# Performance work log

Hardware: AMD Instinct MI355X
Metric: run time of the kernel (lower is better)

## Reference

```python
import jax, jax.numpy as jnp
import numpy as np

NC = 512   # number of symbols / clusters
K = 5      # symbolic conv kernel
S = 2      # symbolic conv stride


def _patches(img, k, s):
    """Extract kxk windows with stride s. img: (H,W) or (H,W,C) int symbols.
    Returns (oh, ow, k, k[, C])."""
    H, W = img.shape[0], img.shape[1]
    oh = (H - k) // s + 1
    ow = (W - k) // s + 1
    hi = jnp.arange(oh) * s
    wi = jnp.arange(ow) * s
    r = img[hi[:, None, None, None] + jnp.arange(k)[None, None, :, None],
            wi[None, :, None, None] + jnp.arange(k)[None, None, None, :]]
    return r, oh, ow


def _sym_conv(sym_img, weights, conv_lut, add_lut):
    """Symbolic conv: per-window gather into conv_lut, sort symbols, then
    sequential left-fold through add_lut (as in SymConv2D).
    sym_img: (H,W) or (H,W,C) int symbols; weights: (L, F) with L=k*k*C."""
    win, oh, ow = _patches(sym_img, K, S)
    if win.ndim == 5:  # (oh,ow,k,k,C) -> channel-major per-window vector (matches reshape(w//C, h*C))
        win = jnp.moveaxis(win, -1, 2)  # (oh,ow,C,k,k)
    win = win.reshape(oh * ow, -1)                      # (n, L)
    prod = conv_lut[win[:, None, :], weights.T[None, :, :]]  # (n, F, L)
    srt = jnp.sort(prod, axis=-1)
    xs = jnp.moveaxis(srt[..., 1:], -1, 0)              # (L-1, n, F)

    def step(carry, s):
        return add_lut[s, carry], None

    out, _ = jax.lax.scan(step, srt[..., 0], xs)        # (n, F)
    return out.reshape(oh, ow, -1)


def _forward_one(x, centroid_lut, W1, W2, W3, conv_lut, add_lut, relu_lut, c1_w, c2_w):
    # discretize: nearest-centroid symbol per 1x1 patch (emulates faiss index)
    sym = jnp.argmin(jnp.abs(x[..., None] - centroid_lut[None, None, :]), axis=-1)  # (28,28)
    h = _sym_conv(sym, c1_w, conv_lut, add_lut)   # (12,12,8)
    h = relu_lut[h]
    h = _sym_conv(h, c2_w, conv_lut, add_lut)     # (4,4,16)
    h = relu_lut[h]
    v = centroid_lut[h]                           # symbolic -> real, (4,4,16)
    v = jnp.transpose(v, (2, 0, 1)).reshape(-1)   # permute(2,0,1).reshape(256)
    a = jax.nn.relu(v @ W1.T)
    a = jax.nn.relu(a @ W2.T)
    return jax.nn.softmax(a @ W3.T)


def setup_inputs() -> dict:
    key = jax.random.key(0)
    ks = jax.random.split(key, 10)
    B = 2048
    return {
        "x_bat": jax.random.uniform(ks[0], (B, 1, 28, 28), jnp.float32),
        "centroid_lut": jax.random.normal(ks[1], (NC,), jnp.float32),
        "W1": jax.random.normal(ks[2], (128, 256), jnp.float32) * 0.06,
        "W2": jax.random.normal(ks[3], (64, 128), jnp.float32) * 0.09,
        "W3": jax.random.normal(ks[4], (10, 64), jnp.float32) * 0.12,
        "conv_lut": jax.random.randint(ks[5], (NC, NC), 0, NC, jnp.int32),
        "add_lut": jax.random.randint(ks[6], (NC, NC), 0, NC, jnp.int32),
        "relu_lut": jax.random.randint(ks[7], (NC,), 0, NC, jnp.int32),
        "c1_weights": jax.random.randint(ks[8], (25, 8), 0, NC, jnp.int32),
        "c2_weights": jax.random.randint(ks[9], (200, 16), 0, NC, jnp.int32),
    }


def reference(x_bat, centroid_lut, W1, W2, W3, conv_lut, add_lut, relu_lut,
              c1_weights, c2_weights):
    f = lambda img: _forward_one(img, centroid_lut, W1, W2, W3,
                                 conv_lut, add_lut, relu_lut,
                                 c1_weights, c2_weights)
    return jax.vmap(f)(x_bat[:, 0])  # (B, 10)
```

## Files before the change

kernel.cpp:

```cpp
#include <hip/hip_runtime.h>


__global__ __launch_bounds__(256) void k_prep(const int* __restrict__ conv_lut,
                                              const int* __restrict__ add_lut,
                                              const int* __restrict__ relu_lut,
                                              unsigned short* __restrict__ lutT,
                                              unsigned short* __restrict__ add16,
                                              unsigned short* __restrict__ relu16) {
  int id = blockIdx.x * 256 + threadIdx.x;
  int s = id >> 9, c = id & 511;
  lutT[c * 512 + s] = (unsigned short)conv_lut[id];
  add16[id] = (unsigned short)add_lut[id];
  if (id < 512) relu16[id] = (unsigned short)relu_lut[id];
}

__global__ __launch_bounds__(256) void k_quant(const float* __restrict__ x,
                                               const float* __restrict__ cen,
                                               unsigned short* __restrict__ sym) {
  __shared__ float cs[512];
  int t = threadIdx.x;
  cs[t] = cen[t];
  cs[t + 256] = cen[t + 256];
  __syncthreads();
  int pix = blockIdx.x * 256 + t;
  float xv = x[pix];
  float bd = 1e30f;
  int bi = 0;
  #pragma unroll 8
  for (int j = 0; j < 512; ++j) {
    float d = fabsf(xv - cs[j]);
    if (d < bd) { bd = d; bi = j; }
  }
  sym[pix] = (unsigned short)bi;
}

__global__ __launch_bounds__(64) void k_conv1(const unsigned short* __restrict__ sym,
                                              const int* __restrict__ c1w,
                                              const unsigned short* __restrict__ lutT,
                                              const unsigned short* __restrict__ add16,
                                              const unsigned short* __restrict__ relu16,
                                              unsigned short* __restrict__ h1) {
  int bid = blockIdx.x;
  int f = bid / 4608;
  int chunk = bid - f * 4608;
  int W = chunk * 64 + threadIdx.x;
  int i = W / 144;
  int p = W - i * 144;
  int wr = p / 12;
  int wc = p - wr * 12;
  const unsigned short* sp = sym + i * 784 + (2 * wr) * 28 + 2 * wc;

  unsigned v[32];
  #pragma unroll
  for (int kh = 0; kh < 5; ++kh)
    #pragma unroll
    for (int kw = 0; kw < 5; ++kw) {
      int l = kh * 5 + kw;
      unsigned sy = sp[kh * 28 + kw];
      int wt = c1w[l * 8 + f];
      v[l] = lutT[((unsigned)wt << 9) + sy];
    }
  #pragma unroll
  for (int l = 25; l < 32; ++l) v[l] = 0xFFFFFFFFu;

  #pragma unroll
  for (int k = 2; k <= 32; k <<= 1) {
    #pragma unroll
    for (int j = k >> 1; j > 0; j >>= 1) {
      #pragma unroll
      for (int a = 0; a < 32; ++a) {
        int b = a ^ j;
        if (b > a) {
          unsigned x0 = v[a], x1 = v[b];
          unsigned lo = min(x0, x1), hi = max(x0, x1);
          bool up = ((a & k) == 0);
          v[a] = up ? lo : hi;
          v[b] = up ? hi : lo;
        }
      }
    }
  }

  unsigned carry = v[0];
  #pragma unroll 1
  for (int l = 1; l < 25; ++l)
    carry = add16[(v[l] << 9) + carry];
  h1[((i * 8 + f) * 12 + wr) * 12 + wc] = relu16[carry];
}

__global__ __launch_bounds__(64) void k_conv2(const unsigned short* __restrict__ h1,
                                              const int* __restrict__ c2w,
                                              const unsigned short* __restrict__ lutT,
                                              const unsigned short* __restrict__ add16,
                                              const unsigned short* __restrict__ relu16,
                                              unsigned short* __restrict__ h2) {
  __shared__ unsigned hist[64][64];
  int lane = threadIdx.x;
  int bid = blockIdx.x;
  int f = bid >> 9;
  int chunk = bid & 511;
  int W = chunk * 64 + lane;
  int i = W >> 4;
  int p = W & 15;
  int wr = p >> 2, wc = p & 3;

  #pragma unroll
  for (int w = 0; w < 64; ++w) hist[w][lane] = 0;

  #pragma unroll 1
  for (int c = 0; c < 8; ++c) {
    int base = ((i * 8 + c) * 12 + 2 * wr) * 12 + 2 * wc;
    #pragma unroll
    for (int kh = 0; kh < 5; ++kh)
      #pragma unroll
      for (int kw = 0; kw < 5; ++kw) {
        unsigned sy = h1[base + kh * 12 + kw];
        int wt = c2w[(c * 25 + kh * 5 + kw) * 16 + f];
        unsigned prod = lutT[((unsigned)wt << 9) + sy];
        hist[prod >> 3][lane] += 1u << ((prod & 7) << 2);
      }
  }

  int wptr = 0;
  unsigned cur = hist[0][lane];
  while (cur == 0 && wptr < 63) { ++wptr; cur = hist[wptr][lane]; }
  unsigned tz = __builtin_ctz(cur);
  unsigned nb = tz >> 2;
  unsigned carry = wptr * 8 + nb;
  cur -= 1u << (nb << 2);
  #pragma unroll 1
  for (int j = 1; j < 200; ++j) {
    while (cur == 0 && wptr < 63) { ++wptr; cur = hist[wptr][lane]; }
    tz = __builtin_ctz(cur);
    nb = tz >> 2;
    unsigned s = wptr * 8 + nb;
    cur -= 1u << (nb << 2);
    carry = add16[(s << 9) + carry];
  }
  h2[((i * 16 + f) * 4 + wr) * 4 + wc] = relu16[carry];
}

__global__ __launch_bounds__(128) void k_mlp(const unsigned short* __restrict__ h2,
                                             const float* __restrict__ cen,
                                             const float* __restrict__ W1,
                                             const float* __restrict__ W2,
                                             const float* __restrict__ W3,
                                             float* __restrict__ out) {
  __shared__ float v[256];
  __shared__ float a1[128];
  __shared__ float a2[64];
  __shared__ float lg[10];
  int i = blockIdx.x, t = threadIdx.x;
  v[t] = cen[h2[i * 256 + t]];
  v[t + 128] = cen[h2[i * 256 + t + 128]];
  __syncthreads();
  float acc = 0.f;
  #pragma unroll 4
  for (int k = 0; k < 256; ++k) acc = fmaf(W1[t * 256 + k], v[k], acc);
  a1[t] = fmaxf(acc, 0.f);
  __syncthreads();
  if (t < 64) {
    acc = 0.f;
    #pragma unroll 4
    for (int k = 0; k < 128; ++k) acc = fmaf(W2[t * 128 + k], a1[k], acc);
    a2[t] = fmaxf(acc, 0.f);
  }
  __syncthreads();
  if (t < 10) {
    acc = 0.f;
    #pragma unroll
    for (int k = 0; k < 64; ++k) acc = fmaf(W3[t * 64 + k], a2[k], acc);
    lg[t] = acc;
  }
  __syncthreads();
  if (t < 10) {
    float m = lg[0];
    #pragma unroll
    for (int j = 1; j < 10; ++j) m = fmaxf(m, lg[j]);
    float ssum = 0.f;
    #pragma unroll
    for (int j = 0; j < 10; ++j) ssum += expf(lg[j] - m);
    out[i * 10 + t] = expf(lg[t] - m) / ssum;
  }
}

extern "C" void kernel_launch(void* const* d_in, const int* in_sizes, int n_in,
                              void* d_out, int out_size, void* d_ws, size_t ws_size,
                              hipStream_t stream) {
  const float* x    = (const float*)d_in[0];
  const float* cen  = (const float*)d_in[1];
  const float* W1   = (const float*)d_in[2];
  const float* W2   = (const float*)d_in[3];
  const float* W3   = (const float*)d_in[4];
  const int* conv_lut = (const int*)d_in[5];
  const int* add_lut  = (const int*)d_in[6];
  const int* relu_lut = (const int*)d_in[7];
  const int* c1w = (const int*)d_in[8];
  const int* c2w = (const int*)d_in[9];
  float* out = (float*)d_out;

  char* ws = (char*)d_ws;
  unsigned short* lutT   = (unsigned short*)(ws);
  unsigned short* add16  = (unsigned short*)(ws + 524288);
  unsigned short* relu16 = (unsigned short*)(ws + 1048576);
  unsigned short* sym    = (unsigned short*)(ws + 1052672);
  unsigned short* h1     = (unsigned short*)(ws + 4263936);
  unsigned short* h2     = (unsigned short*)(ws + 8982528);

  hipLaunchKernelGGL(k_prep,  dim3(1024),  dim3(256), 0, stream,
                     conv_lut, add_lut, relu_lut, lutT, add16, relu16);
  hipLaunchKernelGGL(k_quant, dim3(6272),  dim3(256), 0, stream, x, cen, sym);
  hipLaunchKernelGGL(k_conv1, dim3(36864), dim3(64),  0, stream,
                     sym, c1w, lutT, add16, relu16, h1);
  hipLaunchKernelGGL(k_conv2, dim3(8192),  dim3(64),  0, stream,
                     h1, c2w, lutT, add16, relu16, h2);
  hipLaunchKernelGGL(k_mlp,   dim3(2048),  dim3(128), 0, stream,
                     h2, cen, W1, W2, W3, out);
}
```

Measured before the change: 815.9 us.

## Make conv2 fold wave-synchronous by symbol value; quantize two pixels per thread

The conv2 sorted-fold loop now walks symbol values 0..511 in lockstep across the wavefront. All lanes that hold the same next symbol read the same add_lut row together, which is meant to improve locality of the table gathers. This adds a wave-wide ballot loop over all 512 values, costing up to 512 plus 200 iterations per lane. The quantize kernel also handles two pixels per thread with half the blocks, so each shared centroid load is reused twice.

Result: slower. 1.636 ms (+100.5%).

```diff
diff --git a/kernel.cpp b/kernel.cpp
--- a/kernel.cpp
+++ b/kernel.cpp
@@ -23,15 +23,20 @@
   cs[t + 256] = cen[t + 256];
   __syncthreads();
   int pix = blockIdx.x * 256 + t;
-  float xv = x[pix];
-  float bd = 1e30f;
-  int bi = 0;
+  const int HALF = 802816;
+  float x1 = x[pix], x2 = x[pix + HALF];
+  float b1 = 1e30f, b2 = 1e30f;
+  int i1 = 0, i2 = 0;
   #pragma unroll 8
   for (int j = 0; j < 512; ++j) {
-    float d = fabsf(xv - cs[j]);
-    if (d < bd) { bd = d; bi = j; }
-  }
-  sym[pix] = (unsigned short)bi;
+    float c = cs[j];
+    float d1 = fabsf(x1 - c);
+    float d2 = fabsf(x2 - c);
+    if (d1 < b1) { b1 = d1; i1 = j; }
+    if (d2 < b2) { b2 = d2; i2 = j; }
+  }
+  sym[pix] = (unsigned short)i1;
+  sym[pix + HALF] = (unsigned short)i2;
 }
 
 __global__ __launch_bounds__(64) void k_conv1(const unsigned short* __restrict__ sym,
@@ -124,18 +129,22 @@
   int wptr = 0;
   unsigned cur = hist[0][lane];
   while (cur == 0 && wptr < 63) { ++wptr; cur = hist[wptr][lane]; }
-  unsigned tz = __builtin_ctz(cur);
-  unsigned nb = tz >> 2;
-  unsigned carry = wptr * 8 + nb;
-  cur -= 1u << (nb << 2);
+  unsigned nextv = wptr * 8u + (__builtin_ctz(cur) >> 2);
+  unsigned carry = 0;
+  bool first = true;
+
   #pragma unroll 1
-  for (int j = 1; j < 200; ++j) {
-    while (cur == 0 && wptr < 63) { ++wptr; cur = hist[wptr][lane]; }
-    tz = __builtin_ctz(cur);
-    nb = tz >> 2;
-    unsigned s = wptr * 8 + nb;
-    cur -= 1u << (nb << 2);
-    carry = add16[(s << 9) + carry];
+  for (unsigned r = 0; r < 512; ++r) {
+    while (__any(nextv == r)) {
+      if (nextv == r) {
+        carry = first ? r : (unsigned)add16[(r << 9) + carry];
+        first = false;
+        unsigned sh = ((__builtin_ctz(cur) >> 2) << 2);
+        cur -= 1u << sh;
+        while (cur == 0 && wptr < 63) { ++wptr; cur = hist[wptr][lane]; }
+        nextv = cur ? (wptr * 8u + (__builtin_ctz(cur) >> 2)) : 0xFFFFu;
+      }
+    }
   }
   h2[((i * 16 + f) * 4 + wr) * 4 + wc] = relu16[carry];
 }
@@ -209,7 +218,7 @@
 
   hipLaunchKernelGGL(k_prep,  dim3(1024),  dim3(256), 0, stream,
                      conv_lut, add_lut, relu_lut, lutT, add16, relu16);
-  hipLaunchKernelGGL(k_quant, dim3(6272),  dim3(256), 0, stream, x, cen, sym);
+  hipLaunchKernelGGL(k_quant, dim3(3136),  dim3(256), 0, stream, x, cen, sym);
   hipLaunchKernelGGL(k_conv1, dim3(36864), dim3(64),  0, stream,
                      sym, c1w, lutT, add16, relu16, h1);
   hipLaunchKernelGGL(k_conv2, dim3(8192),  dim3(64),  0, stream,
```
